# Kernel tuning notes

Hardware: AMD Instinct MI355X
Metric: run time of the kernel (lower is better)

Reference implementation:

```python
import jax, jax.numpy as jnp
import numpy as np

THETA_ALPHA = 160.0  # spatial bandwidth of bilateral kernel
THETA_BETA = 3.0     # color bandwidth of bilateral kernel
THETA_GAMMA = 3.0    # spatial bandwidth of spatial kernel
NUM_ITERS = 5        # mean-field iterations


def setup_inputs() -> dict:
    key = jax.random.key(0)
    ks = jax.random.split(key, 5)
    B, H, W, C = 1, 80, 80, 21
    unaries = jax.random.normal(ks[0], (B, H, W, C), dtype=jnp.float32)
    image = jax.random.uniform(ks[1], (B, H, W, 3), dtype=jnp.float32) * 255.0
    spatial_w = jax.random.normal(ks[2], (C, C), dtype=jnp.float32) * 0.1 + jnp.eye(C)
    bilateral_w = jax.random.normal(ks[3], (C, C), dtype=jnp.float32) * 0.1 + jnp.eye(C)
    compat = jax.random.normal(ks[4], (C, C), dtype=jnp.float32) * 0.1 - jnp.eye(C)
    return {"unaries": unaries, "image": image, "spatial_w": spatial_w,
            "bilateral_w": bilateral_w, "compat": compat}


def _gauss_kernel(feat):
    # feat: [N, F] -> dense Gaussian affinity exp(-0.5*||f_i - f_j||^2), [N, N]
    sq = jnp.sum(feat * feat, axis=-1)
    d2 = sq[:, None] + sq[None, :] - 2.0 * (feat @ feat.T)
    return jnp.exp(-0.5 * jnp.maximum(d2, 0.0))


def reference(unaries, image, spatial_w, bilateral_w, compat):
    B, H, W, C = unaries.shape
    N = H * W
    yy, xx = jnp.meshgrid(jnp.arange(H, dtype=jnp.float32),
                          jnp.arange(W, dtype=jnp.float32), indexing="ij")
    pos = jnp.stack([yy, xx], axis=-1).reshape(N, 2)          # [N, 2]
    rgb = image.reshape(N, 3)
    feat_s = pos / THETA_GAMMA                                 # spatial kernel features
    feat_b = jnp.concatenate([pos / THETA_ALPHA, rgb / THETA_BETA], axis=-1)
    Ks = _gauss_kernel(feat_s)                                 # [N, N]
    Kb = _gauss_kernel(feat_b)                                 # [N, N]
    norm_s = jnp.sum(Ks, axis=-1, keepdims=True)               # splat-of-ones normalization
    norm_b = jnp.sum(Kb, axis=-1, keepdims=True)
    u = unaries.reshape(N, C)
    q = u
    for _ in range(NUM_ITERS):
        p = jax.nn.softmax(q, axis=-1)                         # [N, C]
        msg = (Ks @ p) / norm_s @ spatial_w.T + (Kb @ p) / norm_b @ bilateral_w.T
        q = u - msg @ compat.T                                 # compatibility transform
    return q.reshape(B, H, W, C)
```

## Files before the change

kernel.cpp:

```cpp
#include <hip/hip_runtime.h>


#define HH 80
#define WW 80
#define NPIX 6400
#define CC 21
#define PP 24
#define NITER 5
#define NCAP 32
#define SADGATE 23u
#define RAD 14

typedef short short8 __attribute__((ext_vector_type(8)));
union H8 { short8 v; unsigned short u[8]; };
union U4 { uint4 v; unsigned u[4]; };

__device__ __forceinline__ float bf2f(unsigned short h) {
    return __uint_as_float(((unsigned)h) << 16);
}
__device__ __forceinline__ unsigned short f2bf(float f) {
    unsigned u = __float_as_uint(f);
    return (unsigned short)((u + 0x7fffu + ((u >> 16) & 1u)) >> 16);
}

__global__ void __launch_bounds__(1024) nbr_kernel(const float* __restrict__ image,
        const float* __restrict__ unaries,
        const float* __restrict__ sw, const float* __restrict__ bw,
        const float* __restrict__ ct,
        unsigned* __restrict__ nbr_pk, int* __restrict__ nbr_cnt,
        float* __restrict__ inv_ns_g, float* __restrict__ csw_g, float* __restrict__ cbw_g,
        unsigned short* __restrict__ p0) {
    __shared__ unsigned int cimg[NPIX];
    __shared__ float Sl[HH];
    __shared__ int   njl[16][NCAP];
    __shared__ float nkl[16][NCAP];
    int tid = threadIdx.x;
    int bid = blockIdx.x;
    for (int px = tid; px < NPIX; px += 1024) {
        float r = image[px * 3 + 0], g = image[px * 3 + 1], b = image[px * 3 + 2];
        unsigned ur = (unsigned)(r + 0.5f), ug = (unsigned)(g + 0.5f), ub = (unsigned)(b + 0.5f);
        cimg[px] = ur | (ug << 8) | (ub << 16);
    }
    if (tid < HH) {
        float s = 0.f;
        float t = (float)tid;
        for (int tp = 0; tp < HH; ++tp) {
            float d = t - (float)tp;
            s += __expf(-d * d * (1.0f / 18.0f));
        }
        Sl[tid] = s;
    }
    if (bid == 0) {
        for (int idx = tid; idx < 2 * CC * CC; idx += 1024) {
            int m = idx % (CC * CC);
            int c = m / CC, k = m % CC;
            const float* wmat = (idx < CC * CC) ? sw : bw;
            float s = 0.f;
            for (int mm = 0; mm < CC; ++mm) s += ct[c * CC + mm] * wmat[mm * CC + k];
            if (idx < CC * CC) csw_g[m] = s; else cbw_g[m] = s;
        }
    }
    __syncthreads();
    int lane = tid & 63;
    int w = tid >> 6;
    int i = bid * 16 + w;
    unsigned ci = cimg[i];
    float eir = image[i * 3 + 0], eig = image[i * 3 + 1], eib = image[i * 3 + 2];
    float yi = (float)(i / WW), xi = (float)(i % WW);
    int base = 0;
    float ksum = 0.f;
    const uint4* cimg4 = (const uint4*)cimg;
    for (int j0 = 0; j0 < NPIX; j0 += 256) {
        U4 cj4; cj4.v = cimg4[(j0 >> 2) + lane];
        #pragma unroll
        for (int q = 0; q < 4; ++q) {
            int j = j0 + lane * 4 + q;
            unsigned cj = cj4.u[q];
#if __has_builtin(__builtin_amdgcn_sad_u8)
            unsigned sad = __builtin_amdgcn_sad_u8(ci, cj, 0u);
#else
            int dr = (int)(ci & 255u) - (int)(cj & 255u);
            int dg = (int)((ci >> 8) & 255u) - (int)((cj >> 8) & 255u);
            int db = (int)((ci >> 16) & 255u) - (int)((cj >> 16) & 255u);
            unsigned sad = (unsigned)(abs(dr) + abs(dg) + abs(db));
#endif
            bool pass = (sad <= SADGATE);
            unsigned long long mask = __ballot(pass);
            if (pass) {
                int slot = base + __popcll(mask & ((1ull << lane) - 1ull));
                if (slot < NCAP) {
                    float er = eir - image[j * 3 + 0];
                    float eg = eig - image[j * 3 + 1];
                    float eb = eib - image[j * 3 + 2];
                    float dy = (yi - (float)(j / WW)) * (1.0f / 160.0f);
                    float dx = (xi - (float)(j % WW)) * (1.0f / 160.0f);
                    float d2 = (er * er + eg * eg + eb * eb) * (1.0f / 9.0f) + dy * dy + dx * dx;
                    float kk = __expf(-0.5f * d2);
                    njl[w][slot] = j;
                    nkl[w][slot] = kk;
                    ksum += kk;
                }
            }
            base += (int)__popcll(mask);
        }
    }
    for (int off = 32; off > 0; off >>= 1) ksum += __shfl_down(ksum, off, 64);
    ksum = __shfl(ksum, 0, 64);
    int cnt = (base < NCAP) ? base : NCAP;
    float inv = 1.0f / ksum;
    if (lane < cnt) {
        unsigned kk16 = (unsigned)f2bf(nkl[w][lane] * inv);
        nbr_pk[i * NCAP + lane] = ((unsigned)njl[w][lane] << 16) | kk16;
    }
    if (lane == 0) {
        nbr_cnt[i] = cnt;
        inv_ns_g[i] = 1.0f / (Sl[(int)yi] * Sl[(int)xi]);
    }
    float v = (lane < CC) ? unaries[i * CC + lane] : -1e30f;
    float m = v;
    for (int off = 16; off > 0; off >>= 1) m = fmaxf(m, __shfl_down(m, off, 32));
    m = __shfl(m, 0, 32);
    float e = (lane < CC) ? __expf(v - m) : 0.f;
    float s = e;
    for (int off = 16; off > 0; off >>= 1) s += __shfl_down(s, off, 32);
    s = __shfl(s, 0, 32);
    if (lane < PP) p0[i * PP + lane] = (lane < CC) ? f2bf(e / s) : (unsigned short)0;
}

__global__ void __launch_bounds__(256) iter_kernel(const float* __restrict__ unaries,
        const unsigned short* __restrict__ pc,
        const unsigned* __restrict__ nbr_pk, const int* __restrict__ nbr_cnt,
        const float* __restrict__ inv_ns_g,
        const float* __restrict__ csw_g, const float* __restrict__ cbw_g,
        unsigned short* __restrict__ pn, float* __restrict__ out, int last) {
    __shared__ float lcsw[CC * CC], lcbw[CC * CC];
    __shared__ float gl[16];
    __shared__ float cy[2][36 * PP];

    int tid = threadIdx.x;
    int y = blockIdx.x / 10;
    int x0 = (blockIdx.x % 10) * 8;
    int xs = (x0 - RAD > 0) ? x0 - RAD : 0;
    int xe = (x0 + 8 + RAD < WW) ? x0 + 8 + RAD : WW;
    int extw = xe - xs;
    const short8* pc8 = (const short8*)pc;

    int px = tid >> 5, c = tid & 31;
    int x = x0 + px;
    int i = y * WW + x;

    int   cnt = nbr_cnt[i];
    unsigned pk = 0;
    if (c < cnt) pk = nbr_pk[i * NCAP + c];
    float inv_ns = inv_ns_g[i];
    float u_i = (c < CC) ? unaries[i * CC + c] : 0.f;

    for (int idx = tid; idx < 2 * CC * CC; idx += 256) {
        if (idx < CC * CC) lcsw[idx] = csw_g[idx];
        else lcbw[idx - CC * CC] = cbw_g[idx - CC * CC];
    }
    if (tid < 16) { float d = (float)tid; gl[tid] = __expf(-d * d * (1.0f / 18.0f)); }
    if (tid < extw * 6) {
        int col = tid / 6, sub = tid % 6;
        int grp = sub >> 1, half = sub & 1;
        int xa = xs + col;
        int ys_ = (y - RAD > 0) ? y - RAD : 0;
        int ye_ = (y + RAD < HH - 1) ? y + RAD : HH - 1;
        float a[8] = {0, 0, 0, 0, 0, 0, 0, 0};
        for (int yp = ys_ + half; yp <= ye_; yp += 2) {
            float d = (float)(y - yp);
            float g = __expf(-d * d * (1.0f / 18.0f));
            H8 h; h.v = pc8[(yp * WW + xa) * 3 + grp];
            #pragma unroll
            for (int e = 0; e < 8; ++e) a[e] += g * bf2f(h.u[e]);
        }
        #pragma unroll
        for (int e = 0; e < 8; ++e) cy[half][col * PP + grp * 8 + e] = a[e];
    }
    __syncthreads();

    float as_v = 0.f;
    if (c < CC) {
        int q0 = (x - RAD > 0) ? x - RAD : 0;
        int q1 = (x + RAD < WW - 1) ? x + RAD : WW - 1;
        float s = 0.f;
        for (int xp = q0; xp <= q1; ++xp) {
            int d = x - xp; if (d < 0) d = -d;
            int a = (xp - xs) * PP + c;
            s += gl[d] * (cy[0][a] + cy[1][a]);
        }
        as_v = s * inv_ns;
    }
    float ab_v = 0.f;
    for (int n = 0; n < cnt; ++n) {
        unsigned pkn = __shfl(pk, n, 32);
        int jn = (int)(pkn >> 16);
        float kn = bf2f((unsigned short)(pkn & 0xffffu));
        if (c < CC) ab_v += kn * bf2f(pc[jn * PP + c]);
    }
    float m = 0.f;
    #pragma unroll
    for (int k = 0; k < CC; ++k) {
        float ak = __shfl(as_v, k, 32);
        float bk = __shfl(ab_v, k, 32);
        if (c < CC) m += lcsw[c * CC + k] * ak + lcbw[c * CC + k] * bk;
    }
    if (last) {
        if (c < CC) out[i * CC + c] = u_i - m;
    } else {
        float ev = (c < CC) ? __expf(u_i - m) : 0.f;
        float s = ev;
        #pragma unroll
        for (int off = 16; off > 0; off >>= 1) s += __shfl_xor(s, off, 32);
        if (c < PP) pn[i * PP + c] = f2bf(ev / s);
    }
}

extern "C" void kernel_launch(void* const* d_in, const int* in_sizes, int n_in,
                              void* d_out, int out_size, void* d_ws, size_t ws_size,
                              hipStream_t stream) {
    const float* unaries = (const float*)d_in[0];
    const float* image   = (const float*)d_in[1];
    const float* sw      = (const float*)d_in[2];
    const float* bw      = (const float*)d_in[3];
    const float* ct      = (const float*)d_in[4];
    float* out = (float*)d_out;

    char* ws = (char*)d_ws;
    size_t off = 0;
    auto alloc = [&](size_t bytes) -> char* {
        char* p = ws + off;
        off += (bytes + 255) & ~(size_t)255;
        return p;
    };
    unsigned* nbr_pk = (unsigned*)alloc((size_t)NPIX * NCAP * 4);
    int*   nbr_cnt   = (int*)alloc((size_t)NPIX * 4);
    float* inv_ns_g  = (float*)alloc((size_t)NPIX * 4);
    unsigned short* pA = (unsigned short*)alloc((size_t)NPIX * PP * 2 + 256);
    unsigned short* pB = (unsigned short*)alloc((size_t)NPIX * PP * 2 + 256);
    float* csw_g   = (float*)alloc(CC * CC * 4);
    float* cbw_g   = (float*)alloc(CC * CC * 4);
    (void)ws_size;

    nbr_kernel<<<400, 1024, 0, stream>>>(image, unaries, sw, bw, ct,
                                         nbr_pk, nbr_cnt, inv_ns_g,
                                         csw_g, cbw_g, pA);
    unsigned short* pc = pA;
    unsigned short* pn = pB;
    for (int t = 0; t < NITER; ++t) {
        iter_kernel<<<800, 256, 0, stream>>>(unaries, pc, nbr_pk, nbr_cnt,
                                             inv_ns_g, csw_g, cbw_g, pn, out,
                                             (t == NITER - 1) ? 1 : 0);
        unsigned short* tsw = pc; pc = pn; pn = tsw;
    }
}
```

Baseline: 140.3 us.

## Shrink spatial radius, skip empty SAD chunks, register mixing weights, remap blocks

Several changes land together. The spatial Gaussian truncation radius drops from 14 to 10, which cuts the column-sum and row-sum work and shrinks shared memory. The neighbor search now skips a 256-pixel chunk with a single ballot when no lane's SAD passes the gate. The compat-mixed weight rows are held in per-thread registers instead of shared memory, blocks are remapped into row bands, and the bilateral gather loop is unrolled by two with dual accumulators. A radius of 10 at sigma 3 drops tails of about exp(-5.6) relative weight, which slightly changes accuracy.

After: 131.1 us (median of 2 runs). 1.07x faster.

```diff
diff --git a/kernel.cpp b/kernel.cpp
--- a/kernel.cpp
+++ b/kernel.cpp
@@ -9,7 +9,7 @@
 #define NITER 5
 #define NCAP 32
 #define SADGATE 23u
-#define RAD 14
+#define RAD 10
 
 typedef short short8 __attribute__((ext_vector_type(8)));
 union H8 { short8 v; unsigned short u[8]; };
@@ -72,19 +72,25 @@
     const uint4* cimg4 = (const uint4*)cimg;
     for (int j0 = 0; j0 < NPIX; j0 += 256) {
         U4 cj4; cj4.v = cimg4[(j0 >> 2) + lane];
+        unsigned sd[4];
         #pragma unroll
         for (int q = 0; q < 4; ++q) {
-            int j = j0 + lane * 4 + q;
+#if __has_builtin(__builtin_amdgcn_sad_u8)
+            sd[q] = __builtin_amdgcn_sad_u8(ci, cj4.u[q], 0u);
+#else
             unsigned cj = cj4.u[q];
-#if __has_builtin(__builtin_amdgcn_sad_u8)
-            unsigned sad = __builtin_amdgcn_sad_u8(ci, cj, 0u);
-#else
             int dr = (int)(ci & 255u) - (int)(cj & 255u);
             int dg = (int)((ci >> 8) & 255u) - (int)((cj >> 8) & 255u);
             int db = (int)((ci >> 16) & 255u) - (int)((cj >> 16) & 255u);
-            unsigned sad = (unsigned)(abs(dr) + abs(dg) + abs(db));
+            sd[q] = (unsigned)(abs(dr) + abs(dg) + abs(db));
 #endif
-            bool pass = (sad <= SADGATE);
+        }
+        unsigned smin = min(min(sd[0], sd[1]), min(sd[2], sd[3]));
+        if (__ballot(smin <= SADGATE) == 0ull) continue;
+        #pragma unroll
+        for (int q = 0; q < 4; ++q) {
+            int j = j0 + lane * 4 + q;
+            bool pass = (sd[q] <= SADGATE);
             unsigned long long mask = __ballot(pass);
             if (pass) {
                 int slot = base + __popcll(mask & ((1ull << lane) - 1ull));
@@ -133,13 +139,14 @@
         const float* __restrict__ inv_ns_g,
         const float* __restrict__ csw_g, const float* __restrict__ cbw_g,
         unsigned short* __restrict__ pn, float* __restrict__ out, int last) {
-    __shared__ float lcsw[CC * CC], lcbw[CC * CC];
     __shared__ float gl[16];
-    __shared__ float cy[2][36 * PP];
+    __shared__ float cy[2][28 * PP];
 
     int tid = threadIdx.x;
-    int y = blockIdx.x / 10;
-    int x0 = (blockIdx.x % 10) * 8;
+    int band = blockIdx.x & 7;
+    int local = blockIdx.x >> 3;
+    int y = band * 10 + local / 10;
+    int x0 = (local % 10) * 8;
     int xs = (x0 - RAD > 0) ? x0 - RAD : 0;
     int xe = (x0 + 8 + RAD < WW) ? x0 + 8 + RAD : WW;
     int extw = xe - xs;
@@ -149,16 +156,17 @@
     int x = x0 + px;
     int i = y * WW + x;
 
+    float wsw[CC], wbw[CC];
+    if (c < CC) {
+        #pragma unroll
+        for (int k = 0; k < CC; ++k) { wsw[k] = csw_g[c * CC + k]; wbw[k] = cbw_g[c * CC + k]; }
+    }
     int   cnt = nbr_cnt[i];
     unsigned pk = 0;
     if (c < cnt) pk = nbr_pk[i * NCAP + c];
     float inv_ns = inv_ns_g[i];
     float u_i = (c < CC) ? unaries[i * CC + c] : 0.f;
 
-    for (int idx = tid; idx < 2 * CC * CC; idx += 256) {
-        if (idx < CC * CC) lcsw[idx] = csw_g[idx];
-        else lcbw[idx - CC * CC] = cbw_g[idx - CC * CC];
-    }
     if (tid < 16) { float d = (float)tid; gl[tid] = __expf(-d * d * (1.0f / 18.0f)); }
     if (tid < extw * 6) {
         int col = tid / 6, sub = tid % 6;
@@ -191,19 +199,31 @@
         }
         as_v = s * inv_ns;
     }
-    float ab_v = 0.f;
-    for (int n = 0; n < cnt; ++n) {
-        unsigned pkn = __shfl(pk, n, 32);
-        int jn = (int)(pkn >> 16);
-        float kn = bf2f((unsigned short)(pkn & 0xffffu));
-        if (c < CC) ab_v += kn * bf2f(pc[jn * PP + c]);
-    }
+    float ab0 = 0.f, ab1 = 0.f;
+    for (int n = 0; n + 1 < cnt; n += 2) {
+        unsigned pa = __shfl(pk, n, 32);
+        unsigned pb = __shfl(pk, n + 1, 32);
+        int ja = (int)(pa >> 16), jb = (int)(pb >> 16);
+        float ka = bf2f((unsigned short)(pa & 0xffffu));
+        float kb = bf2f((unsigned short)(pb & 0xffffu));
+        if (c < CC) {
+            ab0 += ka * bf2f(pc[ja * PP + c]);
+            ab1 += kb * bf2f(pc[jb * PP + c]);
+        }
+    }
+    if (cnt & 1) {
+        unsigned pa = __shfl(pk, cnt - 1, 32);
+        int ja = (int)(pa >> 16);
+        float ka = bf2f((unsigned short)(pa & 0xffffu));
+        if (c < CC) ab0 += ka * bf2f(pc[ja * PP + c]);
+    }
+    float ab_v = ab0 + ab1;
     float m = 0.f;
     #pragma unroll
     for (int k = 0; k < CC; ++k) {
         float ak = __shfl(as_v, k, 32);
         float bk = __shfl(ab_v, k, 32);
-        if (c < CC) m += lcsw[c * CC + k] * ak + lcbw[c * CC + k] * bk;
+        if (c < CC) m += wsw[k] * ak + wbw[k] * bk;
     }
     if (last) {
         if (c < CC) out[i * CC + c] = u_i - m;
```
